# Performance work log

Measured on AMD Instinct MI355X. Metric: run time of the kernel, lower is better.

The kernel has to match this reference:

```python
import jax, jax.numpy as jnp
import numpy as np

N, E = 100000, 1600000
IN, HID, HEADS, OUT = 128, 16, 4, 64
SLOPE = 0.2  # leaky_relu negative_slope default


def setup_inputs() -> dict:
    key = jax.random.key(0)
    ks = jax.random.split(key, 12)
    s = 0.1  # xavier-ish scale
    return {
        "x": jax.random.normal(ks[0], (N, IN), jnp.float32),
        "edge_index": jax.random.randint(ks[1], (2, E), 0, N, jnp.int32),
        "W1": jax.random.normal(ks[2], (IN, HEADS * HID), jnp.float32) * s,
        "att_l1": jax.random.normal(ks[3], (1, HEADS, HID), jnp.float32) * s,
        "att_r1": jax.random.normal(ks[4], (1, HEADS, HID), jnp.float32) * s,
        "res_W1": jax.random.normal(ks[5], (IN, HEADS * HID), jnp.float32) * s,
        "b1": jnp.zeros((HEADS * HID,), jnp.float32),
        "W2": jax.random.normal(ks[6], (HEADS * HID, OUT), jnp.float32) * s,
        "att_l2": jax.random.normal(ks[7], (1, 1, OUT), jnp.float32) * s,
        "att_r2": jax.random.normal(ks[8], (1, 1, OUT), jnp.float32) * s,
        "b2": jnp.zeros((OUT,), jnp.float32),
    }


def agdn_conv(x, W, att_l, att_r, bias, res_W, src, dst):
    # x: [n, in]; W: [in, H*C]; att_*: [1, H, C]
    n = x.shape[0]
    H, C = att_l.shape[1], att_l.shape[2]
    x_lin = (x @ W).reshape(n, H, C)
    # residual: res_fc if present, else identity on x_lin (residual=True path)
    x_res = (x @ res_W) if res_W is not None else x_lin.reshape(n, H * C)
    al = jnp.sum(x_lin * att_l, axis=-1)  # [n, H]
    ar = jnp.sum(x_lin * att_r, axis=-1)  # [n, H]
    logits = jax.nn.leaky_relu(al[src] + ar[dst], SLOPE)  # [E, H]
    # segment softmax over incoming edges of each dst node
    m = jax.ops.segment_max(logits, dst, num_segments=n)
    e = jnp.exp(logits - m[dst])
    ssum = jax.ops.segment_sum(e, dst, num_segments=n)
    alpha = e / (ssum[dst] + 1e-16)  # [E, H]
    msg = x_lin[src] * alpha[:, :, None]  # [E, H, C]
    out = jax.ops.segment_sum(msg, dst, num_segments=n).reshape(n, H * C)
    return out + x_res + bias


def reference(x, edge_index, W1, att_l1, att_r1, res_W1, b1, W2, att_l2, att_r2, b2):
    src, dst = edge_index[0], edge_index[1]
    h = agdn_conv(x, W1, att_l1, att_r1, b1, res_W1, src, dst)
    h = jax.nn.elu(h)
    # last layer: heads=1, in==heads*out so res_fc is None (residual = x_lin)
    return agdn_conv(h, W2, att_l2, att_r2, b2, None, src, dst)
```

## Files before the change

kernel.cpp:

```cpp
#include <hip/hip_runtime.h>
#include <hip/hip_bf16.h>
#include <hip/hip_fp16.h>
#include <math.h>

#define NN 100000
#define EE 1600000
#define IN_DIM 128
#define HID 16
#define HEADS 4
#define D1 64
#define OUT_DIM 64
#define SLOPE 0.2f

#define NB 391
#define BCAP 5120
#define BINA_CHUNK 4096
#define BINA_BLOCKS ((EE + BINA_CHUNK - 1) / BINA_CHUNK)
#define NODE_BLOCKS ((NN + 63) / 64)
#define AGG_BLOCKS (NN / 16)

#define W1COLS 144
#define LDB1 272
#define LDB2 144

typedef __attribute__((ext_vector_type(8))) short bf16x8;
typedef __attribute__((ext_vector_type(4))) float f32x4;

__device__ __forceinline__ float leaky(float v) { return v > 0.f ? v : SLOPE * v; }
__device__ __forceinline__ unsigned short f2bf(float f) {
    __hip_bfloat16 h = __float2bfloat16(f);
    return *(unsigned short*)&h;
}
__device__ __forceinline__ __half2 u2h2(unsigned u) {
    union { unsigned u; __half2 h; } c; c.u = u; return c.h;
}
__device__ __forceinline__ bf16x8 pack8(float4 a, float4 b) {
    bf16x8 r;
    r[0] = (short)f2bf(a.x); r[1] = (short)f2bf(a.y);
    r[2] = (short)f2bf(a.z); r[3] = (short)f2bf(a.w);
    r[4] = (short)f2bf(b.x); r[5] = (short)f2bf(b.y);
    r[6] = (short)f2bf(b.z); r[7] = (short)f2bf(b.w);
    return r;
}

__global__ __launch_bounds__(256, 4) void node1_kernel(
        const float* __restrict__ x,
        const unsigned short* __restrict__ Wtb,
        const float* __restrict__ b1,
        __half* __restrict__ xlin1h,
        float* __restrict__ acc1,
        float* __restrict__ al1,
        float* __restrict__ ar1) {
    __shared__ char smemB[W1COLS * LDB1];
    int t = threadIdx.x;
    int base = blockIdx.x * 64;
    int wave = t >> 6, lane = t & 63;
    int quad = lane >> 4, li = lane & 15;
    int node = base + wave * 16 + li;

    uint4 breg[9];
#pragma unroll
    for (int s = 0; s < 9; s++) {
        int seg = s * 256 + t;
        breg[s] = *(const uint4*)(Wtb + (seg >> 4) * 128 + (seg & 15) * 8);
    }
    float4 xreg[8];
#pragma unroll
    for (int i = 0; i < 8; i++) xreg[i] = make_float4(0.f, 0.f, 0.f, 0.f);
    if (node < NN) {
        const float* xp = x + (size_t)node * IN_DIM + quad * 8;
#pragma unroll
        for (int kc = 0; kc < 4; kc++) {
            xreg[kc * 2]     = *(const float4*)(xp + kc * 32);
            xreg[kc * 2 + 1] = *(const float4*)(xp + kc * 32 + 4);
        }
    }
#pragma unroll
    for (int s = 0; s < 9; s++) {
        int seg = s * 256 + t;
        *(uint4*)(smemB + (seg >> 4) * LDB1 + (seg & 15) * 16) = breg[s];
    }
    __syncthreads();

    f32x4 accs[9];
#pragma unroll
    for (int nt = 0; nt < 9; nt++) accs[nt] = (f32x4){0.f, 0.f, 0.f, 0.f};
#pragma unroll
    for (int kc = 0; kc < 4; kc++) {
        bf16x8 afrag = pack8(xreg[kc * 2], xreg[kc * 2 + 1]);
        const char* brow = smemB + kc * 64 + quad * 16;
#pragma unroll
        for (int nt = 0; nt < 9; nt++) {
            bf16x8 bfrag = *(const bf16x8*)(brow + (nt * 16 + li) * LDB1);
            accs[nt] = __builtin_amdgcn_mfma_f32_16x16x32_bf16(afrag, bfrag, accs[nt], 0, 0, 0);
        }
    }

    int m0 = base + wave * 16;
#pragma unroll
    for (int nt = 0; nt < 4; nt++) {
#pragma unroll
        for (int j = 0; j < 4; j++) {
            int nd = m0 + quad * 4 + j;
            if (nd < NN) xlin1h[(size_t)nd * D1 + nt * 16 + li] = __float2half(accs[nt][j]);
        }
    }
#pragma unroll
    for (int nt = 4; nt < 8; nt++) {
        int col = (nt - 4) * 16 + li;
        float bv = b1[col];
#pragma unroll
        for (int j = 0; j < 4; j++) {
            int nd = m0 + quad * 4 + j;
            if (nd < NN) acc1[(size_t)nd * D1 + col] = accs[nt][j] + bv;
        }
    }
#pragma unroll
    for (int j = 0; j < 4; j++) {
        int nd = m0 + quad * 4 + j;
        if (nd < NN) {
            if (li < 4) al1[nd * HEADS + li] = accs[8][j];
            else if (li < 8) ar1[nd * HEADS + (li - 4)] = accs[8][j];
        }
    }
}

__global__ void prep_kernel(int* __restrict__ bucket_cursor,
                            const float* __restrict__ W1,
                            const float* __restrict__ resW,
                            const float* __restrict__ W2,
                            const float* __restrict__ attl1,
                            const float* __restrict__ attr1,
                            const float* __restrict__ attl2,
                            const float* __restrict__ attr2,
                            unsigned short* __restrict__ Wtb,
                            unsigned short* __restrict__ W2tb,
                            float* __restrict__ vl, float* __restrict__ vr) {
    int t = threadIdx.x;
    if (blockIdx.x == 0) {
        if (t < NB) bucket_cursor[t] = t * BCAP;
    } else if (blockIdx.x == 1) {
        for (int idx = t; idx < W1COLS * 128; idx += 512) {
            int col = idx >> 7, k = idx & 127;
            float w = 0.f;
            if (col < 64) {
                w = W1[k * 64 + col];
            } else if (col < 128) {
                w = resW[k * 64 + (col - 64)];
            } else if (col < 132) {
                int hh = col - 128;
                for (int c = 0; c < HID; c++)
                    w += W1[k * 64 + hh * HID + c] * attl1[hh * HID + c];
            } else if (col < 136) {
                int hh = col - 132;
                for (int c = 0; c < HID; c++)
                    w += W1[k * 64 + hh * HID + c] * attr1[hh * HID + c];
            }
            Wtb[idx] = f2bf(w);
        }
    } else {
        for (int idx = t; idx < 64 * 64; idx += 512) {
            int col = idx >> 6, k = idx & 63;
            W2tb[idx] = f2bf(W2[k * 64 + col]);
        }
        if (t < D1) {
            float a = 0.f, b = 0.f;
            for (int o = 0; o < OUT_DIM; o++) {
                float w = W2[t * OUT_DIM + o];
                a += w * attl2[o];
                b += w * attr2[o];
            }
            vl[t] = a; vr[t] = b;
        }
    }
}

__global__ __launch_bounds__(256) void binA_kernel(const int* __restrict__ src,
                                                   const int* __restrict__ dst,
                                                   int* __restrict__ bucket_cursor,
                                                   unsigned* __restrict__ binned) {
    __shared__ unsigned spack[BINA_CHUNK];
    __shared__ unsigned short sbkt[BINA_CHUNK];
    __shared__ int lhist[512], lscan[512], gbase[512], lcur[512];
    int t = threadIdx.x;
    lhist[t] = 0; lhist[t + 256] = 0;
    lcur[t] = 0;  lcur[t + 256] = 0;
    __syncthreads();
    int e0 = blockIdx.x * BINA_CHUNK;
    int nvalid = EE - e0; if (nvalid > BINA_CHUNK) nvalid = BINA_CHUNK;
    unsigned pk[16];
    unsigned short bk[16];
#pragma unroll
    for (int i = 0; i < 16; i++) {
        int e = e0 + t + i * 256;
        if (e < EE) {
            int d = dst[e], s = src[e];
            int b = d >> 8;
            pk[i] = ((unsigned)(d & 255) << 24) | (unsigned)s;
            bk[i] = (unsigned short)b;
            atomicAdd(&lhist[b], 1);
        } else bk[i] = 0xFFFFu;
    }
    __syncthreads();
    int c1 = lhist[t], c2 = lhist[t + 256];
    for (int off = 1; off < 512; off <<= 1) {
        int a1 = (t >= off) ? lhist[t - off] : 0;
        int a2 = (t + 256 >= off) ? lhist[t + 256 - off] : 0;
        __syncthreads();
        lhist[t] += a1; lhist[t + 256] += a2;
        __syncthreads();
    }
    lscan[t] = lhist[t] - c1;
    lscan[t + 256] = lhist[t + 256] - c2;
    if (c1) gbase[t] = atomicAdd(&bucket_cursor[t], c1);
    if (c2) gbase[t + 256] = atomicAdd(&bucket_cursor[t + 256], c2);
    __syncthreads();
#pragma unroll
    for (int i = 0; i < 16; i++) {
        if (bk[i] != 0xFFFFu) {
            int b = bk[i];
            int pos = atomicAdd(&lcur[b], 1);
            int slot = lscan[b] + pos;
            spack[slot] = pk[i];
            sbkt[slot] = (unsigned short)b;
        }
    }
    __syncthreads();
    for (int j = t; j < nvalid; j += 256) {
        int b = sbkt[j];
        int idx = gbase[b] + (j - lscan[b]);
        if (idx < (b + 1) * BCAP) binned[idx] = spack[j];
    }
}

__global__ __launch_bounds__(256) void binB_kernel(const unsigned* __restrict__ binned,
                                                   const int* __restrict__ bucket_cursor,
                                                   int* __restrict__ row_ptr,
                                                   int* __restrict__ counts,
                                                   int* __restrict__ sorted_src) {
    __shared__ int lcount[256], lrow[256], lcur[256];
    int b = blockIdx.x, t = threadIdx.x;
    int start = b * BCAP;
    int cnt = bucket_cursor[b] - start;
    if (cnt > BCAP) cnt = BCAP;
    lcount[t] = 0;
    __syncthreads();
    for (int i = t; i < cnt; i += 256) {
        atomicAdd(&lcount[binned[start + i] >> 24], 1);
    }
    __syncthreads();
    int v = lcount[t];
    lrow[t] = v;
    __syncthreads();
    for (int off = 1; off < 256; off <<= 1) {
        int a = (t >= off) ? lrow[t - off] : 0;
        __syncthreads();
        lrow[t] += a;
        __syncthreads();
    }
    int ex = lrow[t] - v;
    __syncthreads();
    lrow[t] = ex;
    lcur[t] = 0;
    int node = (b << 8) + t;
    if (node < NN) {
        row_ptr[node] = start + ex;
        counts[node] = v;
    }
    __syncthreads();
    for (int i = t; i < cnt; i += 256) {
        unsigned p = binned[start + i];
        int low = p >> 24;
        int pos = atomicAdd(&lcur[low], 1);
        sorted_src[start + lrow[low] + pos] = (int)(p & 0xFFFFFFu);
    }
}

__global__ __launch_bounds__(256) void agg1_kernel(
        const int* __restrict__ sorted_src, const int* __restrict__ row_ptr,
        const int* __restrict__ counts,
        const float* __restrict__ al1, const float* __restrict__ ar1,
        const __half* __restrict__ xlin1h, float* __restrict__ acc1,
        const float* __restrict__ vl, const float* __restrict__ vr,
        float* __restrict__ al2, float* __restrict__ ar2) {
    __shared__ __half s_alpha[4][4][64][4];
    __shared__ int    s_src[4][4][64];
    int w = threadIdx.x >> 6, lane = threadIdx.x & 63;
    int g = lane >> 4, li = lane & 15;
    int d = blockIdx.x * 16 + w * 4 + g;
    int rs = row_ptr[d];
    int deg = counts[d];
    const float4 arv = *(const float4*)(ar1 + d * 4);
    int h = li >> 2;

    int maxdeg = deg;
    maxdeg = max(maxdeg, __shfl_xor(maxdeg, 16, 64));
    maxdeg = max(maxdeg, __shfl_xor(maxdeg, 32, 64));
    bool big = maxdeg > 64;

    float s0 = 0.f, s1 = 0.f, s2 = 0.f, s3 = 0.f;
    float ex[4][4];
    int sv[4];
    if (!big) {
#pragma unroll
        for (int it = 0; it < 4; it++) {
            int e = li + it * 16;
            if (e < deg) {
                int s = sorted_src[rs + e];
                sv[it] = s;
                const float4 alv = *(const float4*)(al1 + s * 4);
                ex[it][0] = __expf(leaky(alv.x + arv.x));
                ex[it][1] = __expf(leaky(alv.y + arv.y));
                ex[it][2] = __expf(leaky(alv.z + arv.z));
                ex[it][3] = __expf(leaky(alv.w + arv.w));
                s0 += ex[it][0]; s1 += ex[it][1]; s2 += ex[it][2]; s3 += ex[it][3];
            }
        }
    } else {
        for (int e = li; e < deg; e += 16) {
            int s = sorted_src[rs + e];
            const float4 alv = *(const float4*)(al1 + s * 4);
            s0 += __expf(leaky(alv.x + arv.x));
            s1 += __expf(leaky(alv.y + arv.y));
            s2 += __expf(leaky(alv.z + arv.z));
            s3 += __expf(leaky(alv.w + arv.w));
        }
    }
#pragma unroll
    for (int off = 1; off < 16; off <<= 1) {
        s0 += __shfl_xor(s0, off, 64);
        s1 += __shfl_xor(s1, off, 64);
        s2 += __shfl_xor(s2, off, 64);
        s3 += __shfl_xor(s3, off, 64);
    }
    float inv0 = 1.f / (s0 + 1e-16f), inv1 = 1.f / (s1 + 1e-16f);
    float inv2 = 1.f / (s2 + 1e-16f), inv3 = 1.f / (s3 + 1e-16f);
    if (!big) {
#pragma unroll
        for (int it = 0; it < 4; it++) {
            int e = li + it * 16;
            if (e < deg) {
                *(__half2*)&s_alpha[w][g][e][0] = __floats2half2_rn(ex[it][0] * inv0, ex[it][1] * inv1);
                *(__half2*)&s_alpha[w][g][e][2] = __floats2half2_rn(ex[it][2] * inv2, ex[it][3] * inv3);
                s_src[w][g][e] = sv[it];
            }
        }
    }

    __half2 acc01 = __floats2half2_rn(0.f, 0.f);
    __half2 acc23 = acc01;
    float fb0 = 0.f, fb1 = 0.f, fb2 = 0.f, fb3 = 0.f;
    if (!big) {
        for (int i0 = 0; i0 < maxdeg; i0 += 4) {
            int ss[4]; __half ah[4]; uint2 uu[4];
#pragma unroll
            for (int j = 0; j < 4; j++) {
                int i = i0 + j;
                ah[j] = __float2half(0.f);
                ss[j] = 0;
                if (i < deg) { ss[j] = s_src[w][g][i]; ah[j] = s_alpha[w][g][i][h]; }
            }
#pragma unroll
            for (int j = 0; j < 4; j++) {
                int i = i0 + j;
                uu[j] = make_uint2(0u, 0u);
                if (i < deg) uu[j] = *(const uint2*)(xlin1h + (size_t)ss[j] * D1 + li * 4);
            }
#pragma unroll
            for (int j = 0; j < 4; j++) {
                __half2 a2 = __half2half2(ah[j]);
                acc01 = __hfma2(a2, u2h2(uu[j].x), acc01);
                acc23 = __hfma2(a2, u2h2(uu[j].y), acc23);
            }
        }
    } else {
        float arh = (h == 0) ? arv.x : (h == 1) ? arv.y : (h == 2) ? arv.z : arv.w;
        float invh = (h == 0) ? inv0 : (h == 1) ? inv1 : (h == 2) ? inv2 : inv3;
        for (int i = 0; i < deg; i++) {
            int s = sorted_src[rs + i];
            const float4 alv = *(const float4*)(al1 + s * 4);
            float lv = (h == 0) ? alv.x : (h == 1) ? alv.y : (h == 2) ? alv.z : alv.w;
            float a = __expf(leaky(lv + arh)) * invh;
            uint2 u = *(const uint2*)(xlin1h + (size_t)s * D1 + li * 4);
            float2 x01 = __half22float2(u2h2(u.x));
            float2 x23 = __half22float2(u2h2(u.y));
            fb0 += a * x01.x; fb1 += a * x01.y; fb2 += a * x23.x; fb3 += a * x23.y;
        }
    }
    float2 f01 = __half22float2(acc01);
    float2 f23 = __half22float2(acc23);
    float r0 = f01.x + fb0, r1 = f01.y + fb1, r2 = f23.x + fb2, r3 = f23.y + fb3;
    float* p = acc1 + (size_t)d * D1 + li * 4;
    float4 cur = *(float4*)p;
    cur.x += r0; cur.y += r1; cur.z += r2; cur.w += r3;
    cur.x = cur.x > 0.f ? cur.x : (__expf(cur.x) - 1.f);
    cur.y = cur.y > 0.f ? cur.y : (__expf(cur.y) - 1.f);
    cur.z = cur.z > 0.f ? cur.z : (__expf(cur.z) - 1.f);
    cur.w = cur.w > 0.f ? cur.w : (__expf(cur.w) - 1.f);
    *(float4*)p = cur;
    const float4 vl4 = *(const float4*)(vl + li * 4);
    const float4 vr4 = *(const float4*)(vr + li * 4);
    float pl = cur.x * vl4.x + cur.y * vl4.y + cur.z * vl4.z + cur.w * vl4.w;
    float pr = cur.x * vr4.x + cur.y * vr4.y + cur.z * vr4.z + cur.w * vr4.w;
#pragma unroll
    for (int off = 1; off < 16; off <<= 1) {
        pl += __shfl_xor(pl, off, 64);
        pr += __shfl_xor(pr, off, 64);
    }
    if (li == 0) { al2[d] = pl; ar2[d] = pr; }
}

__global__ __launch_bounds__(256) void node2_kernel(
        const float* __restrict__ h,
        const unsigned short* __restrict__ W2tb,
        const float* __restrict__ b2,
        __half* __restrict__ xlin2h,
        float* __restrict__ out) {
    __shared__ char smemB[64 * LDB2];
    int t = threadIdx.x;
    int base = blockIdx.x * 64;
    int wave = t >> 6, lane = t & 63;
    int quad = lane >> 4, li = lane & 15;
    int node = base + wave * 16 + li;

    uint4 breg[2];
#pragma unroll
    for (int s = 0; s < 2; s++) {
        int seg = s * 256 + t;
        breg[s] = *(const uint4*)(W2tb + (seg >> 3) * 64 + (seg & 7) * 8);
    }
    float4 xreg[4];
#pragma unroll
    for (int i = 0; i < 4; i++) xreg[i] = make_float4(0.f, 0.f, 0.f, 0.f);
    if (node < NN) {
        const float* hp = h + (size_t)node * D1 + quad * 8;
#pragma unroll
        for (int kc = 0; kc < 2; kc++) {
            xreg[kc * 2]     = *(const float4*)(hp + kc * 32);
            xreg[kc * 2 + 1] = *(const float4*)(hp + kc * 32 + 4);
        }
    }
#pragma unroll
    for (int s = 0; s < 2; s++) {
        int seg = s * 256 + t;
        *(uint4*)(smemB + (seg >> 3) * LDB2 + (seg & 7) * 16) = breg[s];
    }
    __syncthreads();

    f32x4 accs[4];
#pragma unroll
    for (int nt = 0; nt < 4; nt++) accs[nt] = (f32x4){0.f, 0.f, 0.f, 0.f};
#pragma unroll
    for (int kc = 0; kc < 2; kc++) {
        bf16x8 afrag = pack8(xreg[kc * 2], xreg[kc * 2 + 1]);
        const char* brow = smemB + kc * 64 + quad * 16;
#pragma unroll
        for (int nt = 0; nt < 4; nt++) {
            bf16x8 bfrag = *(const bf16x8*)(brow + (nt * 16 + li) * LDB2);
            accs[nt] = __builtin_amdgcn_mfma_f32_16x16x32_bf16(afrag, bfrag, accs[nt], 0, 0, 0);
        }
    }

    int m0 = base + wave * 16;
#pragma unroll
    for (int nt = 0; nt < 4; nt++) {
        int col = nt * 16 + li;
        float bv = b2[col];
#pragma unroll
        for (int j = 0; j < 4; j++) {
            int nd = m0 + quad * 4 + j;
            if (nd < NN) {
                float v = accs[nt][j];
                xlin2h[(size_t)nd * OUT_DIM + col] = __float2half(v);
                out[(size_t)nd * OUT_DIM + col] = v + bv;
            }
        }
    }
}

__global__ __launch_bounds__(256) void agg2_kernel(
        const int* __restrict__ sorted_src, const int* __restrict__ row_ptr,
        const int* __restrict__ counts,
        const float* __restrict__ al2, const float* __restrict__ ar2,
        const __half* __restrict__ xlin2h, float* __restrict__ out) {
    __shared__ __half s_alpha[4][4][64];
    __shared__ int    s_src[4][4][64];
    int w = threadIdx.x >> 6, lane = threadIdx.x & 63;
    int g = lane >> 4, li = lane & 15;
    int d = blockIdx.x * 16 + w * 4 + g;
    int rs = row_ptr[d];
    int deg = counts[d];
    float ard = ar2[d];

    int maxdeg = deg;
    maxdeg = max(maxdeg, __shfl_xor(maxdeg, 16, 64));
    maxdeg = max(maxdeg, __shfl_xor(maxdeg, 32, 64));
    bool big = maxdeg > 64;

    float ssum = 0.f;
    float ex[4];
    int sv[4];
    if (!big) {
#pragma unroll
        for (int it = 0; it < 4; it++) {
            int e = li + it * 16;
            if (e < deg) {
                int s = sorted_src[rs + e];
                sv[it] = s;
                ex[it] = __expf(leaky(al2[s] + ard));
                ssum += ex[it];
            }
        }
    } else {
        for (int e = li; e < deg; e += 16) {
            int s = sorted_src[rs + e];
            ssum += __expf(leaky(al2[s] + ard));
        }
    }
#pragma unroll
    for (int off = 1; off < 16; off <<= 1) ssum += __shfl_xor(ssum, off, 64);
    float inv = 1.f / (ssum + 1e-16f);
    if (!big) {
#pragma unroll
        for (int it = 0; it < 4; it++) {
            int e = li + it * 16;
            if (e < deg) {
                s_alpha[w][g][e] = __float2half(ex[it] * inv);
                s_src[w][g][e] = sv[it];
            }
        }
    }

    __half2 acc01 = __floats2half2_rn(0.f, 0.f);
    __half2 acc23 = acc01;
    float fb0 = 0.f, fb1 = 0.f, fb2 = 0.f, fb3 = 0.f;
    if (!big) {
        for (int i0 = 0; i0 < maxdeg; i0 += 4) {
            int ss[4]; __half ah[4]; uint2 uu[4];
#pragma unroll
            for (int j = 0; j < 4; j++) {
                int i = i0 + j;
                ah[j] = __float2half(0.f);
                ss[j] = 0;
                if (i < deg) { ss[j] = s_src[w][g][i]; ah[j] = s_alpha[w][g][i]; }
            }
#pragma unroll
            for (int j = 0; j < 4; j++) {
                int i = i0 + j;
                uu[j] = make_uint2(0u, 0u);
                if (i < deg) uu[j] = *(const uint2*)(xlin2h + (size_t)ss[j] * OUT_DIM + li * 4);
            }
#pragma unroll
            for (int j = 0; j < 4; j++) {
                __half2 a2 = __half2half2(ah[j]);
                acc01 = __hfma2(a2, u2h2(uu[j].x), acc01);
                acc23 = __hfma2(a2, u2h2(uu[j].y), acc23);
            }
        }
    } else {
        for (int i = 0; i < deg; i++) {
            int s = sorted_src[rs + i];
            float a = __expf(leaky(al2[s] + ard)) * inv;
            uint2 u = *(const uint2*)(xlin2h + (size_t)s * OUT_DIM + li * 4);
            float2 x01 = __half22float2(u2h2(u.x));
            float2 x23 = __half22float2(u2h2(u.y));
            fb0 += a * x01.x; fb1 += a * x01.y; fb2 += a * x23.x; fb3 += a * x23.y;
        }
    }
    float2 f01 = __half22float2(acc01);
    float2 f23 = __half22float2(acc23);
    float* p = out + (size_t)d * OUT_DIM + li * 4;
    float4 cur = *(float4*)p;
    cur.x += f01.x + fb0; cur.y += f01.y + fb1;
    cur.z += f23.x + fb2; cur.w += f23.y + fb3;
    *(float4*)p = cur;
}

extern "C" void kernel_launch(void* const* d_in, const int* in_sizes, int n_in,
                              void* d_out, int out_size, void* d_ws, size_t ws_size,
                              hipStream_t stream) {
    const float* x     = (const float*)d_in[0];
    const int*   eidx  = (const int*)d_in[1];
    const float* W1    = (const float*)d_in[2];
    const float* attl1 = (const float*)d_in[3];
    const float* attr1 = (const float*)d_in[4];
    const float* resW1 = (const float*)d_in[5];
    const float* b1    = (const float*)d_in[6];
    const float* W2    = (const float*)d_in[7];
    const float* attl2 = (const float*)d_in[8];
    const float* attr2 = (const float*)d_in[9];
    const float* b2    = (const float*)d_in[10];

    const int* src = eidx;
    const int* dst = eidx + EE;

    __half* xlin1h = (__half*)d_ws;
    float* acc1  = (float*)(xlin1h + (size_t)NN * D1);
    float* al1   = acc1 + (size_t)NN * D1;
    float* ar1   = al1 + (size_t)NN * HEADS;
    float* al2   = ar1 + (size_t)NN * HEADS;
    float* ar2   = al2 + NN;
    float* vl    = ar2 + NN;
    float* vr    = vl + D1;
    unsigned short* Wtb  = (unsigned short*)(vr + D1);
    unsigned short* W2tb = Wtb + W1COLS * 128;
    int* counts        = (int*)(W2tb + 64 * 64);
    int* row_ptr       = counts + NN;
    int* bucket_cursor = row_ptr + NN;
    int* sorted_src    = bucket_cursor + 512;
    unsigned* binned = (unsigned*)d_out;
    __half* xlin2h = xlin1h;

    float* out = (float*)d_out;

    prep_kernel<<<3, 512, 0, stream>>>(bucket_cursor, W1, resW1, W2,
                                       attl1, attr1, attl2, attr2,
                                       Wtb, W2tb, vl, vr);
    binA_kernel<<<BINA_BLOCKS, 256, 0, stream>>>(src, dst, bucket_cursor, binned);
    node1_kernel<<<NODE_BLOCKS, 256, 0, stream>>>(x, Wtb, b1,
                                                  xlin1h, acc1, al1, ar1);
    binB_kernel<<<NB, 256, 0, stream>>>(binned, bucket_cursor,
                                        row_ptr, counts, sorted_src);

    agg1_kernel<<<AGG_BLOCKS, 256, 0, stream>>>(sorted_src, row_ptr, counts,
                                                al1, ar1, xlin1h, acc1,
                                                vl, vr, al2, ar2);

    node2_kernel<<<NODE_BLOCKS, 256, 0, stream>>>(acc1, W2tb, b2, xlin2h, out);
    agg2_kernel<<<AGG_BLOCKS, 256, 0, stream>>>(sorted_src, row_ptr, counts,
                                                al2, ar2, xlin2h, out);
}
```

Baseline: 269.4 us.

## Halve intermediate traffic and use 8-lane-per-node aggregation with 16B gathers

```diff
diff --git a/kernel.cpp b/kernel.cpp
--- a/kernel.cpp
+++ b/kernel.cpp
@@ -17,7 +17,7 @@
 #define BINA_CHUNK 4096
 #define BINA_BLOCKS ((EE + BINA_CHUNK - 1) / BINA_CHUNK)
 #define NODE_BLOCKS ((NN + 63) / 64)
-#define AGG_BLOCKS (NN / 16)
+#define AGG_BLOCKS (NN / 32)
 
 #define W1COLS 144
 #define LDB1 272
@@ -48,7 +48,7 @@
         const unsigned short* __restrict__ Wtb,
         const float* __restrict__ b1,
         __half* __restrict__ xlin1h,
-        float* __restrict__ acc1,
+        __half* __restrict__ acc1h,
         float* __restrict__ al1,
         float* __restrict__ ar1) {
     __shared__ char smemB[W1COLS * LDB1];
@@ -112,7 +112,7 @@
 #pragma unroll
         for (int j = 0; j < 4; j++) {
             int nd = m0 + quad * 4 + j;
-            if (nd < NN) acc1[(size_t)nd * D1 + col] = accs[nt][j] + bv;
+            if (nd < NN) acc1h[(size_t)nd * D1 + col] = __float2half(accs[nt][j] + bv);
         }
     }
 #pragma unroll
@@ -280,44 +280,48 @@
         const int* __restrict__ sorted_src, const int* __restrict__ row_ptr,
         const int* __restrict__ counts,
         const float* __restrict__ al1, const float* __restrict__ ar1,
-        const __half* __restrict__ xlin1h, float* __restrict__ acc1,
+        const __half* __restrict__ xlin1h, const __half* __restrict__ acc1h,
+        unsigned short* __restrict__ hb,
         const float* __restrict__ vl, const float* __restrict__ vr,
         float* __restrict__ al2, float* __restrict__ ar2) {
-    __shared__ __half s_alpha[4][4][64][4];
-    __shared__ int    s_src[4][4][64];
+    __shared__ __half s_alpha[4][8][65][4];
+    __shared__ int    s_src[4][8][65];
     int w = threadIdx.x >> 6, lane = threadIdx.x & 63;
-    int g = lane >> 4, li = lane & 15;
-    int d = blockIdx.x * 16 + w * 4 + g;
+    int g = lane >> 3, li = lane & 7;
+    int d = blockIdx.x * 32 + w * 8 + g;
     int rs = row_ptr[d];
     int deg = counts[d];
     const float4 arv = *(const float4*)(ar1 + d * 4);
-    int h = li >> 2;
+    int h = li >> 1;
 
     int maxdeg = deg;
+    maxdeg = max(maxdeg, __shfl_xor(maxdeg, 8, 64));
     maxdeg = max(maxdeg, __shfl_xor(maxdeg, 16, 64));
     maxdeg = max(maxdeg, __shfl_xor(maxdeg, 32, 64));
     bool big = maxdeg > 64;
 
     float s0 = 0.f, s1 = 0.f, s2 = 0.f, s3 = 0.f;
-    float ex[4][4];
-    int sv[4];
     if (!big) {
 #pragma unroll
-        for (int it = 0; it < 4; it++) {
-            int e = li + it * 16;
+        for (int it = 0; it < 8; it++) {
+            int e = li + it * 8;
             if (e < deg) {
                 int s = sorted_src[rs + e];
-                sv[it] = s;
                 const float4 alv = *(const float4*)(al1 + s * 4);
-                ex[it][0] = __expf(leaky(alv.x + arv.x));
-                ex[it][1] = __expf(leaky(alv.y + arv.y));
-                ex[it][2] = __expf(leaky(alv.z + arv.z));
-                ex[it][3] = __expf(leaky(alv.w + arv.w));
-                s0 += ex[it][0]; s1 += ex[it][1]; s2 += ex[it][2]; s3 += ex[it][3];
+                float e0 = __expf(leaky(alv.x + arv.x));
+                float e1 = __expf(leaky(alv.y + arv.y));
+                float e2 = __expf(leaky(alv.z + arv.z));
+                float e3 = __expf(leaky(alv.w + arv.w));
+                s0 += e0; s1 += e1; s2 += e2; s3 += e3;
+                __half2 h01 = __floats2half2_rn(e0, e1);
+                __half2 h23 = __floats2half2_rn(e2, e3);
+                *(uint2*)&s_alpha[w][g][e][0] =
+                    make_uint2(*(unsigned*)&h01, *(unsigned*)&h23);
+                s_src[w][g][e] = s;
             }
         }
     } else {
-        for (int e = li; e < deg; e += 16) {
+        for (int e = li; e < deg; e += 8) {
             int s = sorted_src[rs + e];
             const float4 alv = *(const float4*)(al1 + s * 4);
             s0 += __expf(leaky(alv.x + arv.x));
@@ -327,32 +331,26 @@
         }
     }
 #pragma unroll
-    for (int off = 1; off < 16; off <<= 1) {
+    for (int off = 1; off < 8; off <<= 1) {
         s0 += __shfl_xor(s0, off, 64);
         s1 += __shfl_xor(s1, off, 64);
         s2 += __shfl_xor(s2, off, 64);
         s3 += __shfl_xor(s3, off, 64);
     }
-    float inv0 = 1.f / (s0 + 1e-16f), inv1 = 1.f / (s1 + 1e-16f);
-    float inv2 = 1.f / (s2 + 1e-16f), inv3 = 1.f / (s3 + 1e-16f);
-    if (!big) {
-#pragma unroll
-        for (int it = 0; it < 4; it++) {
-            int e = li + it * 16;
-            if (e < deg) {
-                *(__half2*)&s_alpha[w][g][e][0] = __floats2half2_rn(ex[it][0] * inv0, ex[it][1] * inv1);
-                *(__half2*)&s_alpha[w][g][e][2] = __floats2half2_rn(ex[it][2] * inv2, ex[it][3] * inv3);
-                s_src[w][g][e] = sv[it];
-            }
-        }
-    }
-
-    __half2 acc01 = __floats2half2_rn(0.f, 0.f);
-    __half2 acc23 = acc01;
-    float fb0 = 0.f, fb1 = 0.f, fb2 = 0.f, fb3 = 0.f;
+    float inv0 = 0.f, inv1 = 0.f, inv2 = 0.f, inv3 = 0.f;
+    if (deg > 0) {
+        inv0 = 1.f / (s0 + 1e-16f); inv1 = 1.f / (s1 + 1e-16f);
+        inv2 = 1.f / (s2 + 1e-16f); inv3 = 1.f / (s3 + 1e-16f);
+    }
+    float invh = (h == 0) ? inv0 : (h == 1) ? inv1 : (h == 2) ? inv2 : inv3;
+    __half2 invh2 = __floats2half2_rn(invh, invh);
+
+    __half2 a01 = __floats2half2_rn(0.f, 0.f);
+    __half2 a23 = a01, a45 = a01, a67 = a01;
+    float fb0=0.f, fb1=0.f, fb2=0.f, fb3=0.f, fb4=0.f, fb5=0.f, fb6=0.f, fb7=0.f;
     if (!big) {
         for (int i0 = 0; i0 < maxdeg; i0 += 4) {
-            int ss[4]; __half ah[4]; uint2 uu[4];
+            int ss[4]; __half ah[4]; uint4 uu[4];
 #pragma unroll
             for (int j = 0; j < 4; j++) {
                 int i = i0 + j;
@@ -363,47 +361,68 @@
 #pragma unroll
             for (int j = 0; j < 4; j++) {
                 int i = i0 + j;
-                uu[j] = make_uint2(0u, 0u);
-                if (i < deg) uu[j] = *(const uint2*)(xlin1h + (size_t)ss[j] * D1 + li * 4);
+                uu[j] = make_uint4(0u, 0u, 0u, 0u);
+                if (i < deg) uu[j] = *(const uint4*)(xlin1h + (size_t)ss[j] * D1 + li * 8);
             }
 #pragma unroll
             for (int j = 0; j < 4; j++) {
-                __half2 a2 = __half2half2(ah[j]);
-                acc01 = __hfma2(a2, u2h2(uu[j].x), acc01);
-                acc23 = __hfma2(a2, u2h2(uu[j].y), acc23);
+                __half2 a2 = __hmul2(__half2half2(ah[j]), invh2);
+                a01 = __hfma2(a2, u2h2(uu[j].x), a01);
+                a23 = __hfma2(a2, u2h2(uu[j].y), a23);
+                a45 = __hfma2(a2, u2h2(uu[j].z), a45);
+                a67 = __hfma2(a2, u2h2(uu[j].w), a67);
             }
         }
     } else {
         float arh = (h == 0) ? arv.x : (h == 1) ? arv.y : (h == 2) ? arv.z : arv.w;
-        float invh = (h == 0) ? inv0 : (h == 1) ? inv1 : (h == 2) ? inv2 : inv3;
         for (int i = 0; i < deg; i++) {
             int s = sorted_src[rs + i];
             const float4 alv = *(const float4*)(al1 + s * 4);
             float lv = (h == 0) ? alv.x : (h == 1) ? alv.y : (h == 2) ? alv.z : alv.w;
             float a = __expf(leaky(lv + arh)) * invh;
-            uint2 u = *(const uint2*)(xlin1h + (size_t)s * D1 + li * 4);
+            uint4 u = *(const uint4*)(xlin1h + (size_t)s * D1 + li * 8);
             float2 x01 = __half22float2(u2h2(u.x));
             float2 x23 = __half22float2(u2h2(u.y));
+            float2 x45 = __half22float2(u2h2(u.z));
+            float2 x67 = __half22float2(u2h2(u.w));
             fb0 += a * x01.x; fb1 += a * x01.y; fb2 += a * x23.x; fb3 += a * x23.y;
-        }
-    }
-    float2 f01 = __half22float2(acc01);
-    float2 f23 = __half22float2(acc23);
-    float r0 = f01.x + fb0, r1 = f01.y + fb1, r2 = f23.x + fb2, r3 = f23.y + fb3;
-    float* p = acc1 + (size_t)d * D1 + li * 4;
-    float4 cur = *(float4*)p;
-    cur.x += r0; cur.y += r1; cur.z += r2; cur.w += r3;
-    cur.x = cur.x > 0.f ? cur.x : (__expf(cur.x) - 1.f);
-    cur.y = cur.y > 0.f ? cur.y : (__expf(cur.y) - 1.f);
-    cur.z = cur.z > 0.f ? cur.z : (__expf(cur.z) - 1.f);
-    cur.w = cur.w > 0.f ? cur.w : (__expf(cur.w) - 1.f);
-    *(float4*)p = cur;
-    const float4 vl4 = *(const float4*)(vl + li * 4);
-    const float4 vr4 = *(const float4*)(vr + li * 4);
-    float pl = cur.x * vl4.x + cur.y * vl4.y + cur.z * vl4.z + cur.w * vl4.w;
-    float pr = cur.x * vr4.x + cur.y * vr4.y + cur.z * vr4.z + cur.w * vr4.w;
-#pragma unroll
-    for (int off = 1; off < 16; off <<= 1) {
+            fb4 += a * x45.x; fb5 += a * x45.y; fb6 += a * x67.x; fb7 += a * x67.y;
+        }
+    }
+    float c0, c1, c2, c3, c4, c5, c6, c7;
+    { float2 tv;
+      tv = __half22float2(a01); c0 = tv.x + fb0; c1 = tv.y + fb1;
+      tv = __half22float2(a23); c2 = tv.x + fb2; c3 = tv.y + fb3;
+      tv = __half22float2(a45); c4 = tv.x + fb4; c5 = tv.y + fb5;
+      tv = __half22float2(a67); c6 = tv.x + fb6; c7 = tv.y + fb7; }
+    uint4 rres = *(const uint4*)(acc1h + (size_t)d * D1 + li * 8);
+    { float2 tv;
+      tv = __half22float2(u2h2(rres.x)); c0 += tv.x; c1 += tv.y;
+      tv = __half22float2(u2h2(rres.y)); c2 += tv.x; c3 += tv.y;
+      tv = __half22float2(u2h2(rres.z)); c4 += tv.x; c5 += tv.y;
+      tv = __half22float2(u2h2(rres.w)); c6 += tv.x; c7 += tv.y; }
+    c0 = c0 > 0.f ? c0 : (__expf(c0) - 1.f);
+    c1 = c1 > 0.f ? c1 : (__expf(c1) - 1.f);
+    c2 = c2 > 0.f ? c2 : (__expf(c2) - 1.f);
+    c3 = c3 > 0.f ? c3 : (__expf(c3) - 1.f);
+    c4 = c4 > 0.f ? c4 : (__expf(c4) - 1.f);
+    c5 = c5 > 0.f ? c5 : (__expf(c5) - 1.f);
+    c6 = c6 > 0.f ? c6 : (__expf(c6) - 1.f);
+    c7 = c7 > 0.f ? c7 : (__expf(c7) - 1.f);
+    union { unsigned short us[8]; uint4 u4; } hw;
+    hw.us[0] = f2bf(c0); hw.us[1] = f2bf(c1); hw.us[2] = f2bf(c2); hw.us[3] = f2bf(c3);
+    hw.us[4] = f2bf(c4); hw.us[5] = f2bf(c5); hw.us[6] = f2bf(c6); hw.us[7] = f2bf(c7);
+    *(uint4*)(hb + (size_t)d * D1 + li * 8) = hw.u4;
+    const float4 vla = *(const float4*)(vl + li * 8);
+    const float4 vlb = *(const float4*)(vl + li * 8 + 4);
+    const float4 vra = *(const float4*)(vr + li * 8);
+    const float4 vrb = *(const float4*)(vr + li * 8 + 4);
+    float pl = c0 * vla.x + c1 * vla.y + c2 * vla.z + c3 * vla.w
+             + c4 * vlb.x + c5 * vlb.y + c6 * vlb.z + c7 * vlb.w;
+    float pr = c0 * vra.x + c1 * vra.y + c2 * vra.z + c3 * vra.w
+             + c4 * vrb.x + c5 * vrb.y + c6 * vrb.z + c7 * vrb.w;
+#pragma unroll
+    for (int off = 1; off < 8; off <<= 1) {
         pl += __shfl_xor(pl, off, 64);
         pr += __shfl_xor(pr, off, 64);
     }
@@ -411,11 +430,9 @@
 }
 
 __global__ __launch_bounds__(256) void node2_kernel(
-        const float* __restrict__ h,
+        const unsigned short* __restrict__ hb,
         const unsigned short* __restrict__ W2tb,
-        const float* __restrict__ b2,
-        __half* __restrict__ xlin2h,
-        float* __restrict__ out) {
+        __half* __restrict__ xlin2h) {
     __shared__ char smemB[64 * LDB2];
     int t = threadIdx.x;
     int base = blockIdx.x * 64;
@@ -429,16 +446,14 @@
         int seg = s * 256 + t;
         breg[s] = *(const uint4*)(W2tb + (seg >> 3) * 64 + (seg & 7) * 8);
     }
-    float4 xreg[4];
-#pragma unroll
-    for (int i = 0; i < 4; i++) xreg[i] = make_float4(0.f, 0.f, 0.f, 0.f);
+    bf16x8 afr[2];
+#pragma unroll
+    for (int kc = 0; kc < 2; kc++)
+#pragma unroll
+        for (int i = 0; i < 8; i++) afr[kc][i] = 0;
     if (node < NN) {
-        const float* hp = h + (size_t)node * D1 + quad * 8;
-#pragma unroll
-        for (int kc = 0; kc < 2; kc++) {
-            xreg[kc * 2]     = *(const float4*)(hp + kc * 32);
-            xreg[kc * 2 + 1] = *(const float4*)(hp + kc * 32 + 4);
-        }
+        afr[0] = *(const bf16x8*)(hb + (size_t)node * D1 + quad * 8);
+        afr[1] = *(const bf16x8*)(hb + (size_t)node * D1 + 32 + quad * 8);
     }
 #pragma unroll
     for (int s = 0; s < 2; s++) {
@@ -452,12 +467,11 @@
     for (int nt = 0; nt < 4; nt++) accs[nt] = (f32x4){0.f, 0.f, 0.f, 0.f};
 #pragma unroll
     for (int kc = 0; kc < 2; kc++) {
-        bf16x8 afrag = pack8(xreg[kc * 2], xreg[kc * 2 + 1]);
         const char* brow = smemB + kc * 64 + quad * 16;
 #pragma unroll
         for (int nt = 0; nt < 4; nt++) {
             bf16x8 bfrag = *(const bf16x8*)(brow + (nt * 16 + li) * LDB2);
-            accs[nt] = __builtin_amdgcn_mfma_f32_16x16x32_bf16(afrag, bfrag, accs[nt], 0, 0, 0);
+            accs[nt] = __builtin_amdgcn_mfma_f32_16x16x32_bf16(afr[kc], bfrag, accs[nt], 0, 0, 0);
         }
     }
 
@@ -465,15 +479,10 @@
 #pragma unroll
     for (int nt = 0; nt < 4; nt++) {
         int col = nt * 16 + li;
-        float bv = b2[col];
 #pragma unroll
         for (int j = 0; j < 4; j++) {
             int nd = m0 + quad * 4 + j;
-            if (nd < NN) {
-                float v = accs[nt][j];
-                xlin2h[(size_t)nd * OUT_DIM + col] = __float2half(v);
-                out[(size_t)nd * OUT_DIM + col] = v + bv;
-            }
+            if (nd < NN) xlin2h[(size_t)nd * OUT_DIM + col] = __float2half(accs[nt][j]);
         }
     }
 }
@@ -482,61 +491,53 @@
         const int* __restrict__ sorted_src, const int* __restrict__ row_ptr,
         const int* __restrict__ counts,
         const float* __restrict__ al2, const float* __restrict__ ar2,
-        const __half* __restrict__ xlin2h, float* __restrict__ out) {
-    __shared__ __half s_alpha[4][4][64];
-    __shared__ int    s_src[4][4][64];
+        const __half* __restrict__ xlin2h, const float* __restrict__ b2,
+        float* __restrict__ out) {
+    __shared__ __half s_alpha[4][8][65];
+    __shared__ int    s_src[4][8][65];
     int w = threadIdx.x >> 6, lane = threadIdx.x & 63;
-    int g = lane >> 4, li = lane & 15;
-    int d = blockIdx.x * 16 + w * 4 + g;
+    int g = lane >> 3, li = lane & 7;
+    int d = blockIdx.x * 32 + w * 8 + g;
     int rs = row_ptr[d];
     int deg = counts[d];
     float ard = ar2[d];
 
     int maxdeg = deg;
+    maxdeg = max(maxdeg, __shfl_xor(maxdeg, 8, 64));
     maxdeg = max(maxdeg, __shfl_xor(maxdeg, 16, 64));
     maxdeg = max(maxdeg, __shfl_xor(maxdeg, 32, 64));
     bool big = maxdeg > 64;
 
     float ssum = 0.f;
-    float ex[4];
-    int sv[4];
     if (!big) {
 #pragma unroll
-        for (int it = 0; it < 4; it++) {
-            int e = li + it * 16;
+        for (int it = 0; it < 8; it++) {
+            int e = li + it * 8;
             if (e < deg) {
                 int s = sorted_src[rs + e];
-                sv[it] = s;
-                ex[it] = __expf(leaky(al2[s] + ard));
-                ssum += ex[it];
+                float ex = __expf(leaky(al2[s] + ard));
+                ssum += ex;
+                s_alpha[w][g][e] = __float2half(ex);
+                s_src[w][g][e] = s;
             }
         }
     } else {
-        for (int e = li; e < deg; e += 16) {
+        for (int e = li; e < deg; e += 8) {
             int s = sorted_src[rs + e];
             ssum += __expf(leaky(al2[s] + ard));
         }
     }
 #pragma unroll
-    for (int off = 1; off < 16; off <<= 1) ssum += __shfl_xor(ssum, off, 64);
-    float inv = 1.f / (ssum + 1e-16f);
-    if (!big) {
-#pragma unroll
-        for (int it = 0; it < 4; it++) {
-            int e = li + it * 16;
-            if (e < deg) {
-                s_alpha[w][g][e] = __float2half(ex[it] * inv);
-                s_src[w][g][e] = sv[it];
-            }
-        }
-    }
-
-    __half2 acc01 = __floats2half2_rn(0.f, 0.f);
-    __half2 acc23 = acc01;
-    float fb0 = 0.f, fb1 = 0.f, fb2 = 0.f, fb3 = 0.f;
+    for (int off = 1; off < 8; off <<= 1) ssum += __shfl_xor(ssum, off, 64);
+    float inv = (deg > 0) ? 1.f / (ssum + 1e-16f) : 0.f;
+    __half2 inv2h = __floats2half2_rn(inv, inv);
+
+    __half2 a01 = __floats2half2_rn(0.f, 0.f);
+    __half2 a23 = a01, a45 = a01, a67 = a01;
+    float fb0=0.f, fb1=0.f, fb2=0.f, fb3=0.f, fb4=0.f, fb5=0.f, fb6=0.f, fb7=0.f;
     if (!big) {
         for (int i0 = 0; i0 < maxdeg; i0 += 4) {
-            int ss[4]; __half ah[4]; uint2 uu[4];
+            int ss[4]; __half ah[4]; uint4 uu[4];
 #pragma unroll
             for (int j = 0; j < 4; j++) {
                 int i = i0 + j;
@@ -547,33 +548,50 @@
 #pragma unroll
             for (int j = 0; j < 4; j++) {
                 int i = i0 + j;
-                uu[j] = make_uint2(0u, 0u);
-                if (i < deg) uu[j] = *(const uint2*)(xlin2h + (size_t)ss[j] * OUT_DIM + li * 4);
+                uu[j] = make_uint4(0u, 0u, 0u, 0u);
+                if (i < deg) uu[j] = *(const uint4*)(xlin2h + (size_t)ss[j] * OUT_DIM + li * 8);
             }
 #pragma unroll
             for (int j = 0; j < 4; j++) {
-                __half2 a2 = __half2half2(ah[j]);
-                acc01 = __hfma2(a2, u2h2(uu[j].x), acc01);
-                acc23 = __hfma2(a2, u2h2(uu[j].y), acc23);
+                __half2 a2 = __hmul2(__half2half2(ah[j]), inv2h);
+                a01 = __hfma2(a2, u2h2(uu[j].x), a01);
+                a23 = __hfma2(a2, u2h2(uu[j].y), a23);
+                a45 = __hfma2(a2, u2h2(uu[j].z), a45);
+                a67 = __hfma2(a2, u2h2(uu[j].w), a67);
             }
         }
     } else {
         for (int i = 0; i < deg; i++) {
             int s = sorted_src[rs + i];
             float a = __expf(leaky(al2[s] + ard)) * inv;
-            uint2 u = *(const uint2*)(xlin2h + (size_t)s * OUT_DIM + li * 4);
+            uint4 u = *(const uint4*)(xlin2h + (size_t)s * OUT_DIM + li * 8);
             float2 x01 = __half22float2(u2h2(u.x));
             float2 x23 = __half22float2(u2h2(u.y));
+            float2 x45 = __half22float2(u2h2(u.z));
+            float2 x67 = __half22float2(u2h2(u.w));
             fb0 += a * x01.x; fb1 += a * x01.y; fb2 += a * x23.x; fb3 += a * x23.y;
-        }
-    }
-    float2 f01 = __half22float2(acc01);
-    float2 f23 = __half22float2(acc23);
-    float* p = out + (size_t)d * OUT_DIM + li * 4;
-    float4 cur = *(float4*)p;
-    cur.x += f01.x + fb0; cur.y += f01.y + fb1;
-    cur.z += f23.x + fb2; cur.w += f23.y + fb3;
-    *(float4*)p = cur;
+            fb4 += a * x45.x; fb5 += a * x45.y; fb6 += a * x67.x; fb7 += a * x67.y;
+        }
+    }
+    float c0, c1, c2, c3, c4, c5, c6, c7;
+    { float2 tv;
+      tv = __half22float2(a01); c0 = tv.x + fb0; c1 = tv.y + fb1;
+      tv = __half22float2(a23); c2 = tv.x + fb2; c3 = tv.y + fb3;
+      tv = __half22float2(a45); c4 = tv.x + fb4; c5 = tv.y + fb5;
+      tv = __half22float2(a67); c6 = tv.x + fb6; c7 = tv.y + fb7; }
+    uint4 own = *(const uint4*)(xlin2h + (size_t)d * OUT_DIM + li * 8);
+    { float2 tv;
+      tv = __half22float2(u2h2(own.x)); c0 += tv.x; c1 += tv.y;
+      tv = __half22float2(u2h2(own.y)); c2 += tv.x; c3 += tv.y;
+      tv = __half22float2(u2h2(own.z)); c4 += tv.x; c5 += tv.y;
+      tv = __half22float2(u2h2(own.w)); c6 += tv.x; c7 += tv.y; }
+    const float4 bva = *(const float4*)(b2 + li * 8);
+    const float4 bvb = *(const float4*)(b2 + li * 8 + 4);
+    c0 += bva.x; c1 += bva.y; c2 += bva.z; c3 += bva.w;
+    c4 += bvb.x; c5 += bvb.y; c6 += bvb.z; c7 += bvb.w;
+    float* p = out + (size_t)d * OUT_DIM + li * 8;
+    *(float4*)p = make_float4(c0, c1, c2, c3);
+    *(float4*)(p + 4) = make_float4(c4, c5, c6, c7);
 }
 
 extern "C" void kernel_launch(void* const* d_in, const int* in_sizes, int n_in,
@@ -595,8 +613,9 @@
     const int* dst = eidx + EE;
 
     __half* xlin1h = (__half*)d_ws;
-    float* acc1  = (float*)(xlin1h + (size_t)NN * D1);
-    float* al1   = acc1 + (size_t)NN * D1;
+    __half* acc1h  = xlin1h + (size_t)NN * D1;
+    unsigned short* hb = (unsigned short*)(acc1h + (size_t)NN * D1);
+    float* al1   = (float*)(hb + (size_t)NN * D1);
     float* ar1   = al1 + (size_t)NN * HEADS;
     float* al2   = ar1 + (size_t)NN * HEADS;
     float* ar2   = al2 + NN;
@@ -618,15 +637,15 @@
                                        Wtb, W2tb, vl, vr);
     binA_kernel<<<BINA_BLOCKS, 256, 0, stream>>>(src, dst, bucket_cursor, binned);
     node1_kernel<<<NODE_BLOCKS, 256, 0, stream>>>(x, Wtb, b1,
-                                                  xlin1h, acc1, al1, ar1);
+                                                  xlin1h, acc1h, al1, ar1);
     binB_kernel<<<NB, 256, 0, stream>>>(binned, bucket_cursor,
                                         row_ptr, counts, sorted_src);
 
     agg1_kernel<<<AGG_BLOCKS, 256, 0, stream>>>(sorted_src, row_ptr, counts,
-                                                al1, ar1, xlin1h, acc1,
+                                                al1, ar1, xlin1h, acc1h, hb,
                                                 vl, vr, al2, ar2);
 
-    node2_kernel<<<NODE_BLOCKS, 256, 0, stream>>>(acc1, W2tb, b2, xlin2h, out);
+    node2_kernel<<<NODE_BLOCKS, 256, 0, stream>>>(hb, W2tb, xlin2h);
     agg2_kernel<<<AGG_BLOCKS, 256, 0, stream>>>(sorted_src, row_ptr, counts,
-                                                al2, ar2, xlin2h, out);
-}
+                                                al2, ar2, xlin2h, b2, out);
+}
```

Result: faster. 258.1 us (-4.2%).
